# Kernel optimization log

Measured on AMD Instinct MI355X. Metric: run time of the kernel, lower is better.

The kernel has to match this reference:

```python
import jax, jax.numpy as jnp
import numpy as np

N_USERS = 100000
N_ITEMS = 50001  # item_max + 1 (padding row 0)
N_EDGES = 1000000
D = 64
B = 4096
MAXLEN = 50
NUM_GNN_LAYERS = 2
LAMBDA_A = 0.5


def setup_inputs() -> dict:
    key = jax.random.key(0)
    ks = jax.random.split(key, 11)
    user_table = jax.random.normal(ks[0], (N_USERS, D), jnp.float32) * 0.1
    item_table = jax.random.normal(ks[1], (N_ITEMS, D), jnp.float32) * 0.1
    item_table = item_table.at[0].set(0.0)  # padding_idx=0
    edge_val_uv = jax.random.uniform(ks[2], (N_EDGES,), jnp.float32)
    edge_val_vu = jax.random.uniform(ks[3], (N_EDGES,), jnp.float32)
    W_att_w = jax.random.normal(ks[4], (D, D), jnp.float32) / jnp.sqrt(D)
    W_att_b = jax.random.normal(ks[5], (D,), jnp.float32) * 0.01
    W_agg = jax.random.normal(ks[6], (D, D), jnp.float32) / jnp.sqrt(D)
    edge_u = jax.random.randint(ks[7], (N_EDGES,), 0, N_USERS, jnp.int32)
    edge_i = jax.random.randint(ks[8], (N_EDGES,), 0, N_ITEMS, jnp.int32)
    user_idx = jax.random.randint(ks[9], (B,), 0, N_USERS, jnp.int32)
    ctx_items = jax.random.randint(ks[10], (B, MAXLEN), 0, N_ITEMS, jnp.int32)
    return dict(user_table=user_table, item_table=item_table,
                edge_val_uv=edge_val_uv, edge_val_vu=edge_val_vu,
                W_att_w=W_att_w, W_att_b=W_att_b, W_agg=W_agg,
                edge_u=edge_u, edge_i=edge_i, user_idx=user_idx,
                ctx_items=ctx_items)


def _propagate(V0, edge_u, edge_i, edge_val_uv, edge_val_vu):
    # V_{l+1} = VU @ (UV @ V_l), sparse bipartite spmm via segment sums
    V = V0
    layers = [V]
    for _ in range(NUM_GNN_LAYERS):
        u_msg = jax.ops.segment_sum(edge_val_uv[:, None] * V[edge_i],
                                    edge_u, num_segments=N_USERS)  # [U, D]
        V = jax.ops.segment_sum(edge_val_vu[:, None] * u_msg[edge_u],
                                edge_i, num_segments=N_ITEMS)       # [I, D]
        layers.append(V)
    return jnp.mean(jnp.stack(layers, 0), axis=0) + V0


def reference(user_table, item_table, edge_val_uv, edge_val_vu,
              W_att_w, W_att_b, W_agg,
              edge_u, edge_i, user_idx, ctx_items):
    # item_embedding_select: GNN propagation over bipartite graph
    V = _propagate(item_table, edge_u, edge_i, edge_val_uv, edge_val_vu)

    # forward_user
    id_emb = user_table[user_idx]          # [B, D]
    seq_emb = V[ctx_items]                  # [B, L, D]

    # user_attention_pooling
    key = jnp.tanh(jnp.einsum('bld,ed->ble', seq_emb, W_att_w) + W_att_b)
    attention = jnp.einsum('bld,bd->bl', key, id_emb)
    mask = jnp.sum(seq_emb, axis=-1) == 0   # [B, L]
    X = jnp.where(mask, 0.0, attention)
    eX = jnp.exp(X)
    attn = eX / (jnp.sum(eX, axis=1, keepdims=True) + 1e-12)
    pooled = jnp.einsum('bl,bld->bd', attn, seq_emb)
    out = pooled @ W_agg.T

    return LAMBDA_A * id_emb + (1.0 - LAMBDA_A) * out
```

## Files before the change

kernel.cpp:

```cpp
#include <hip/hip_runtime.h>

#define N_USERS 100000
#define N_ITEMS 50001
#define N_EDGES 1000000
#define D 64
#define BATCH 4096
#define MAXLEN 50

#define SHU 8
#define SHI 7
#define NBU ((N_USERS + 255) >> 8)
#define NBI ((N_ITEMS + 127) >> 7)
#define CAP 3072
#define BEPB 8192
#define BBLOCKS ((N_EDGES + BEPB - 1) / BEPB)

typedef __attribute__((ext_vector_type(8))) short short8;
typedef __attribute__((ext_vector_type(4))) float f32x4;

__device__ __forceinline__ float bf_lo(unsigned u) { return __uint_as_float(u << 16); }
__device__ __forceinline__ float bf_hi(unsigned u) { return __uint_as_float(u & 0xffff0000u); }
__device__ __forceinline__ float bf_s(unsigned short s) { return __uint_as_float(((unsigned)s) << 16); }
__device__ __forceinline__ unsigned bf_pack2(float a, float b) {
    unsigned ba = __float_as_uint(a);
    unsigned bb = __float_as_uint(b);
    ba += 0x7fffu + ((ba >> 16) & 1u);
    bb += 0x7fffu + ((bb >> 16) & 1u);
    return (ba >> 16) | (bb & 0xffff0000u);
}
__device__ __forceinline__ float fast_tanh(float x) {
    float e = __expf(2.0f * x);
    return 1.0f - 2.0f * __builtin_amdgcn_rcpf(e + 1.0f);
}

__global__ __launch_bounds__(256) void convert_kernel(
    const float* __restrict__ src, unsigned* __restrict__ dst, int npairs)
{
    int i = blockIdx.x * 256 + threadIdx.x;
    if (i < npairs) {
        float2 f = ((const float2*)src)[i];
        dst[i] = bf_pack2(f.x, f.y);
    }
}

__global__ __launch_bounds__(512) void bin_kernel(
    const int* __restrict__ eu, const int* __restrict__ ei,
    const float* __restrict__ ev_uv, const float* __restrict__ ev_vu,
    int* __restrict__ gcur_u, int* __restrict__ gcur_i,
    int2* __restrict__ staged_u, int2* __restrict__ staged_i)
{
    __shared__ int hist[NBU];
    __shared__ int runbase[NBU];
    __shared__ unsigned short rank[BEPB];
    int tid = threadIdx.x;
    int dir_i = (blockIdx.x >= BBLOCKS) ? 1 : 0;
    int blk = blockIdx.x - (dir_i ? BBLOCKS : 0);
    const int* erow = dir_i ? ei : eu;
    const int* esrc = dir_i ? eu : ei;
    const float* eval = dir_i ? ev_vu : ev_uv;
    int* gcur = dir_i ? gcur_i : gcur_u;
    int2* staged = dir_i ? staged_i : staged_u;
    const int shift = dir_i ? SHI : SHU;
    const float qs = dir_i ? 32767.0f : 65535.0f;
    const int rlmask = dir_i ? 127 : 255;
    const int nb = dir_i ? NBI : NBU;

    for (int i = tid; i < nb; i += 512) hist[i] = 0;
    __syncthreads();
    int e0 = blk * BEPB;
    for (int k = 0; k < BEPB / 512; ++k) {
        int slot = k * 512 + tid;
        int e = e0 + slot;
        if (e < N_EDGES)
            rank[slot] = (unsigned short)atomicAdd(&hist[erow[e] >> shift], 1);
    }
    __syncthreads();
    for (int i = tid; i < nb; i += 512) {
        int cn = hist[i];
        runbase[i] = cn ? (i * CAP + atomicAdd(&gcur[i], cn)) : 0;
    }
    __syncthreads();
    for (int k = 0; k < BEPB / 512; ++k) {
        int slot = k * 512 + tid;
        int e = e0 + slot;
        if (e < N_EDGES) {
            int row = erow[e];
            unsigned q = (unsigned)(fminf(fmaxf(eval[e], 0.0f), 1.0f) * qs + 0.5f);
            int2 en;
            en.x = (int)((unsigned)(row & rlmask) << 16 | q);
            en.y = esrc[e];
            staged[runbase[row >> shift] + rank[slot]] = en;
        }
    }
}

__global__ __launch_bounds__(512) void place_kernel(
    const int2* __restrict__ staged_u, const int2* __restrict__ staged_i,
    const int* __restrict__ gcur_u, const int* __restrict__ gcur_i,
    unsigned* __restrict__ csr_u, unsigned* __restrict__ csr_i,
    int2* __restrict__ offend_u, int2* __restrict__ offend_i)
{
    __shared__ int cnt[256];
    __shared__ int s[256];
    __shared__ int cur[256];
    int tid = threadIdx.x;
    int dir_i = (blockIdx.x >= NBU) ? 1 : 0;
    int b = blockIdx.x - (dir_i ? NBU : 0);
    const int2* staged = dir_i ? staged_i : staged_u;
    const int* gcur = dir_i ? gcur_i : gcur_u;
    unsigned* csr = dir_i ? csr_i : csr_u;
    int2* offend = dir_i ? offend_i : offend_u;
    const int NR = dir_i ? 128 : 256;
    const int nrows = dir_i ? N_ITEMS : N_USERS;
    const int idxbits = dir_i ? 17 : 16;

    int sb = b * CAP;
    int eb = sb + gcur[b];
    if (tid < NR) cnt[tid] = 0;
    __syncthreads();
    for (int idx = sb + tid; idx < eb; idx += 512) {
        int rl = ((unsigned)staged[idx].x) >> 16;
        atomicAdd(&cnt[rl], 1);
    }
    __syncthreads();
    int c = 0;
    if (tid < 256) {
        c = (tid < NR) ? cnt[tid] : 0;
        s[tid] = c;
    }
    __syncthreads();
    for (int off = 1; off < 256; off <<= 1) {
        int v = 0;
        if (tid >= off && tid < 256) v = s[tid - off];
        __syncthreads();
        if (tid < 256) s[tid] += v;
        __syncthreads();
    }
    if (tid < NR) {
        int excl = s[tid] - c;
        int row = b * NR + tid;
        if (row < nrows) {
            int2 oe; oe.x = sb + excl; oe.y = sb + excl + c;
            offend[row] = oe;
        }
        cur[tid] = sb + excl;
    }
    __syncthreads();
    for (int idx = sb + tid; idx < eb; idx += 512) {
        int2 en = staged[idx];
        unsigned w0 = (unsigned)en.x;
        int rl = w0 >> 16;
        unsigned q = w0 & 0xFFFFu;
        int pos = atomicAdd(&cur[rl], 1);
        csr[pos] = (q << idxbits) | (unsigned)en.y;
    }
}

template<int IDXBITS>
__device__ __forceinline__ void gather_row_g8(
    const unsigned* __restrict__ src, const unsigned* __restrict__ csr,
    int o, int e, int c4, int g,
    float& A0, float& A1, float& A2, float& A3,
    float& A4, float& A5, float& A6, float& A7)
{
    constexpr unsigned MASK = (1u << IDXBITS) - 1u;
    constexpr float SCALE = 1.0f / (float)((1u << (32 - IDXBITS)) - 1u);
    float a0 = 0.f, a1 = 0.f, a2 = 0.f, a3 = 0.f;
    float a4 = 0.f, a5 = 0.f, a6 = 0.f, a7 = 0.f;
    for (int base = o; base < e; base += 8) {
        unsigned word = __builtin_nontemporal_load(csr + base + c4);
        uint4 u4[8];
        float v[8];
#pragma unroll
        for (int j = 0; j < 8; ++j) {
            unsigned wj = (unsigned)__shfl((int)word, 8 * g + j, 64);
            bool valid = (base + j) < e;
            int r = valid ? (int)(wj & MASK) : 0;
            v[j] = valid ? (float)(wj >> IDXBITS) * SCALE : 0.0f;
            u4[j] = *(const uint4*)(src + (size_t)r * 32 + 4 * c4);
        }
#pragma unroll
        for (int j = 0; j < 8; ++j) {
            a0 = fmaf(v[j], bf_lo(u4[j].x), a0);
            a1 = fmaf(v[j], bf_hi(u4[j].x), a1);
            a2 = fmaf(v[j], bf_lo(u4[j].y), a2);
            a3 = fmaf(v[j], bf_hi(u4[j].y), a3);
            a4 = fmaf(v[j], bf_lo(u4[j].z), a4);
            a5 = fmaf(v[j], bf_hi(u4[j].z), a5);
            a6 = fmaf(v[j], bf_lo(u4[j].w), a6);
            a7 = fmaf(v[j], bf_hi(u4[j].w), a7);
        }
    }
    A0 = a0; A1 = a1; A2 = a2; A3 = a3;
    A4 = a4; A5 = a5; A6 = a6; A7 = a7;
}

template<int IDXBITS>
__global__ __launch_bounds__(256) void gather_bf_kernel(
    const unsigned* __restrict__ src, const unsigned* __restrict__ csr,
    const int2* __restrict__ offend,
    unsigned* __restrict__ dst, int nrows)
{
    int gw = (blockIdx.x * 256 + threadIdx.x) >> 6;
    int lane = threadIdx.x & 63;
    int g = lane >> 3, c4 = lane & 7;
    int row = gw * 8 + g;
    int2 oe = (row < nrows) ? offend[row] : make_int2(0, 0);
    float a0, a1, a2, a3, a4, a5, a6, a7;
    gather_row_g8<IDXBITS>(src, csr, oe.x, oe.y, c4, g,
                           a0, a1, a2, a3, a4, a5, a6, a7);
    if (row < nrows) {
        uint4 o4;
        o4.x = bf_pack2(a0, a1);
        o4.y = bf_pack2(a2, a3);
        o4.z = bf_pack2(a4, a5);
        o4.w = bf_pack2(a6, a7);
        *((uint4*)(dst + (size_t)row * 32) + c4) = o4;
    }
}

__global__ __launch_bounds__(256) void gather_final_bf_kernel(
    const unsigned* __restrict__ src, const unsigned* __restrict__ csr,
    const int2* __restrict__ offend,
    const float* __restrict__ V0, const unsigned* __restrict__ V1bf,
    unsigned* __restrict__ Vf_bf)
{
    int gw = (blockIdx.x * 256 + threadIdx.x) >> 6;
    int lane = threadIdx.x & 63;
    int g = lane >> 3, c4 = lane & 7;
    int row = gw * 8 + g;
    int2 oe = (row < N_ITEMS) ? offend[row] : make_int2(0, 0);
    float a0, a1, a2, a3, a4, a5, a6, a7;
    gather_row_g8<17>(src, csr, oe.x, oe.y, c4, g,
                      a0, a1, a2, a3, a4, a5, a6, a7);
    if (row < N_ITEMS) {
        float4 v0a = *((const float4*)(V0 + (size_t)row * 64) + 2 * c4);
        float4 v0b = *((const float4*)(V0 + (size_t)row * 64) + 2 * c4 + 1);
        uint4 u1 = *((const uint4*)(V1bf + (size_t)row * 32) + c4);
        float r0 = (v0a.x + bf_lo(u1.x) + a0) * (1.0f / 3.0f) + v0a.x;
        float r1 = (v0a.y + bf_hi(u1.x) + a1) * (1.0f / 3.0f) + v0a.y;
        float r2 = (v0a.z + bf_lo(u1.y) + a2) * (1.0f / 3.0f) + v0a.z;
        float r3 = (v0a.w + bf_hi(u1.y) + a3) * (1.0f / 3.0f) + v0a.w;
        float r4 = (v0b.x + bf_lo(u1.z) + a4) * (1.0f / 3.0f) + v0b.x;
        float r5 = (v0b.y + bf_hi(u1.z) + a5) * (1.0f / 3.0f) + v0b.y;
        float r6 = (v0b.z + bf_lo(u1.w) + a6) * (1.0f / 3.0f) + v0b.z;
        float r7 = (v0b.w + bf_hi(u1.w) + a7) * (1.0f / 3.0f) + v0b.w;
        uint4 o4;
        o4.x = bf_pack2(r0, r1);
        o4.y = bf_pack2(r2, r3);
        o4.z = bf_pack2(r4, r5);
        o4.w = bf_pack2(r6, r7);
        *((uint4*)(Vf_bf + (size_t)row * 32) + c4) = o4;
    }
}

__global__ __launch_bounds__(256) void phase2_kernel(
    const float* __restrict__ user_table, const unsigned* __restrict__ Vf_bf,
    const float* __restrict__ Watt, const float* __restrict__ Wb,
    const float* __restrict__ Wagg, const int* __restrict__ uidx,
    const int* __restrict__ ctx, float* __restrict__ out)
{
    __shared__ __align__(16) unsigned seq[4][50 * 36];
    __shared__ unsigned short wgT[64 * 65];
    __shared__ __align__(16) float idrow[4][64];
    __shared__ float attn_l[4][64];
    __shared__ float pooled_l[4][64];

    const int tid = threadIdx.x;
    const int w = tid >> 6;
    const int lane = tid & 63;
    const int q = lane >> 4;
    const int n = lane & 15;
    const int b = blockIdx.x * 4 + w;

    int ci = (lane < MAXLEN) ? ctx[b * MAXLEN + lane] : 0;
    const int g8 = lane >> 3, c4v = lane & 7;
    uint4 vv[7];
#pragma unroll
    for (int bt = 0; bt < 7; ++bt) {
        int l = bt * 8 + g8;
        int rsrc = __shfl(ci, l, 64);
        vv[bt] = *((const uint4*)(Vf_bf + (size_t)rsrc * 32) + c4v);
    }

    for (int i = tid; i < 64 * 64; i += 256) {
        int e = i >> 6, d = i & 63;
        unsigned bb = __float_as_uint(Wagg[i]);
        bb += 0x7fffu + ((bb >> 16) & 1u);
        wgT[d * 65 + e] = (unsigned short)(bb >> 16);
    }
    __syncthreads();

    short8 wa_f[4][2];
#pragma unroll
    for (int et = 0; et < 4; ++et)
#pragma unroll
        for (int ks = 0; ks < 2; ++ks) {
            const float* rp = Watt + (size_t)(16 * et + n) * 64 + 32 * ks + 8 * q;
            float4 f0 = *(const float4*)rp;
            float4 f1 = *(const float4*)(rp + 4);
            union { short8 s; unsigned u[4]; } t;
            t.u[0] = bf_pack2(f0.x, f0.y);
            t.u[1] = bf_pack2(f0.z, f0.w);
            t.u[2] = bf_pack2(f1.x, f1.y);
            t.u[3] = bf_pack2(f1.z, f1.w);
            wa_f[et][ks] = t.s;
        }
    f32x4 biasv[4];
#pragma unroll
    for (int et = 0; et < 4; ++et)
        biasv[et] = *(const f32x4*)(Wb + 16 * et + 4 * q);
    short8 ones8;
#pragma unroll
    for (int j = 0; j < 8; ++j) ones8[j] = (short)0x3F80;

    int uid = uidx[b];
    idrow[w][lane] = user_table[(size_t)uid * 64 + lane];
    f32x4 idv[4];
#pragma unroll
    for (int et = 0; et < 4; ++et)
        idv[et] = *(f32x4*)&idrow[w][16 * et + 4 * q];

#pragma unroll
    for (int bt = 0; bt < 7; ++bt) {
        int l = bt * 8 + g8;
        if (l < MAXLEN)
            *(uint4*)&seq[w][l * 36 + 4 * c4v] = vv[bt];
    }

    float xs[4];
#pragma unroll
    for (int lt = 0; lt < 4; ++lt) {
        union { short8 s; uint4 u; } B0, B1;
        B0.u = *(const uint4*)&seq[w][(16 * lt + n) * 36 + 4 * q];
        B1.u = *(const uint4*)&seq[w][(16 * lt + n) * 36 + 16 + 4 * q];

        f32x4 rsum = {0.f, 0.f, 0.f, 0.f};
        rsum = __builtin_amdgcn_mfma_f32_16x16x32_bf16(ones8, B0.s, rsum, 0, 0, 0);
        rsum = __builtin_amdgcn_mfma_f32_16x16x32_bf16(ones8, B1.s, rsum, 0, 0, 0);
        float rsv = rsum[0];

        float xacc = 0.0f;
#pragma unroll
        for (int et = 0; et < 4; ++et) {
            f32x4 a = {0.f, 0.f, 0.f, 0.f};
            a = __builtin_amdgcn_mfma_f32_16x16x32_bf16(wa_f[et][0], B0.s, a, 0, 0, 0);
            a = __builtin_amdgcn_mfma_f32_16x16x32_bf16(wa_f[et][1], B1.s, a, 0, 0, 0);
#pragma unroll
            for (int r = 0; r < 4; ++r) {
                float t = fast_tanh(a[r] + biasv[et][r]);
                xacc = fmaf(t, idv[et][r], xacc);
            }
        }
        xacc += __shfl_xor(xacc, 16, 64);
        xacc += __shfl_xor(xacc, 32, 64);
        xs[lt] = (rsv == 0.0f) ? 0.0f : xacc;
    }

    float ex[4];
    float tot = 0.0f;
#pragma unroll
    for (int lt = 0; lt < 4; ++lt) {
        int l = 16 * lt + n;
        ex[lt] = (l < MAXLEN) ? __expf(xs[lt]) : 0.0f;
        tot += ex[lt];
    }
    tot += __shfl_xor(tot, 1, 64);
    tot += __shfl_xor(tot, 2, 64);
    tot += __shfl_xor(tot, 4, 64);
    tot += __shfl_xor(tot, 8, 64);
    float inv = 1.0f / (tot + 1e-12f);
    if (lane < 16) {
#pragma unroll
        for (int lt = 0; lt < 4; ++lt)
            attn_l[w][16 * lt + lane] = ex[lt] * inv;
    }

    float pooled = 0.0f;
    for (int l = 0; l < MAXLEN; ++l) {
        float a = attn_l[w][l];
        unsigned uu = seq[w][l * 36 + (lane >> 1)];
        float sv = (lane & 1) ? bf_hi(uu) : bf_lo(uu);
        pooled = fmaf(a, sv, pooled);
    }
    pooled_l[w][lane] = pooled;

    float o = 0.0f;
#pragma unroll 8
    for (int d = 0; d < 64; ++d) {
        float pv = pooled_l[w][d];
        float wv = bf_s(wgT[d * 65 + lane]);
        o = fmaf(pv, wv, o);
    }
    out[(size_t)b * 64 + lane] = 0.5f * idrow[w][lane] + 0.5f * o;
}


extern "C" void kernel_launch(void* const* d_in, const int* in_sizes, int n_in,
                              void* d_out, int out_size, void* d_ws, size_t ws_size,
                              hipStream_t stream)
{
    const float* user_table = (const float*)d_in[0];
    const float* item_table = (const float*)d_in[1];
    const float* ev_uv      = (const float*)d_in[2];
    const float* ev_vu      = (const float*)d_in[3];
    const float* Watt       = (const float*)d_in[4];
    const float* Wb         = (const float*)d_in[5];
    const float* Wagg       = (const float*)d_in[6];
    const int*   edge_u     = (const int*)d_in[7];
    const int*   edge_i     = (const int*)d_in[8];
    const int*   uidx       = (const int*)d_in[9];
    const int*   ctx        = (const int*)d_in[10];
    float* out = (float*)d_out;

    const size_t NCAP = (size_t)NBU * CAP;

    char* p = (char*)d_ws;
    unsigned* it_bf    = (unsigned*)p; p += (size_t)N_ITEMS * 32 * 4;
    unsigned* u_msg_bf = (unsigned*)p; p += (size_t)N_USERS * 32 * 4;
    unsigned* V1_bf    = (unsigned*)p; p += (size_t)N_ITEMS * 32 * 4;
    char*     Sreg     = p;            p += NCAP * 8 * 2;
    int2*     staged_u = (int2*)Sreg;
    int2*     staged_i = (int2*)(Sreg + NCAP * 8);
    unsigned* Vf_bf    = (unsigned*)Sreg;
    unsigned* csr_u    = (unsigned*)p; p += NCAP * 4;
    unsigned* csr_i    = (unsigned*)p; p += NCAP * 4;
    int2*     offend_u = (int2*)p;     p += (size_t)N_USERS * 8;
    int2*     offend_i = (int2*)p;     p += (size_t)N_ITEMS * 8;
    int*      gcur_u   = (int*)p;      p += NBU * 4;
    int*      gcur_i   = (int*)p;      p += NBI * 4;

    hipMemsetAsync(gcur_u, 0, (NBU + NBI) * 4, stream);

    convert_kernel<<<(N_ITEMS * 32 + 255) / 256, 256, 0, stream>>>(
        item_table, it_bf, N_ITEMS * 32);

    bin_kernel<<<2 * BBLOCKS, 512, 0, stream>>>(edge_u, edge_i, ev_uv, ev_vu,
                                                gcur_u, gcur_i, staged_u, staged_i);
    place_kernel<<<NBU + NBI, 512, 0, stream>>>(staged_u, staged_i, gcur_u, gcur_i,
                                                csr_u, csr_i, offend_u, offend_i);

    const int ublocks = (N_USERS + 31) / 32;
    const int iblocks = (N_ITEMS + 31) / 32;

    gather_bf_kernel<16><<<ublocks, 256, 0, stream>>>(it_bf, csr_u, offend_u, u_msg_bf, N_USERS);
    gather_bf_kernel<17><<<iblocks, 256, 0, stream>>>(u_msg_bf, csr_i, offend_i, V1_bf, N_ITEMS);
    gather_bf_kernel<16><<<ublocks, 256, 0, stream>>>(V1_bf, csr_u, offend_u, u_msg_bf, N_USERS);
    gather_final_bf_kernel<<<iblocks, 256, 0, stream>>>(u_msg_bf, csr_i, offend_i,
                                                        item_table, V1_bf, Vf_bf);

    phase2_kernel<<<BATCH / 4, 256, 0, stream>>>(user_table, Vf_bf, Watt, Wb, Wagg,
                                                 uidx, ctx, out);
}
```

Before: 254.3 us.

## Split CSR rows into source-index chunks to localize gather accesses

The place kernel now buckets each row's edges by source-index range: 2 chunks for user rows and 4 for item rows. Offsets are stored per (row, chunk), and the gather kernels walk the chunks in order. All rows then touch a similar slice of the source table at roughly the same time, which is meant to improve L2/cache locality of the random embedding gathers. The costs are larger offset arrays, partially filled 8-edge groups at every chunk boundary, and a wider 512-entry scan in place_kernel. Phase2 also moves its context-row gather later, after the weight setup, which lowers register pressure but exposes that load's latency.

```diff
diff --git a/kernel.cpp b/kernel.cpp
--- a/kernel.cpp
+++ b/kernel.cpp
@@ -14,6 +14,11 @@
 #define CAP 3072
 #define BEPB 8192
 #define BBLOCKS ((N_EDGES + BEPB - 1) / BEPB)
+
+#define NCH_U 2
+#define NCH_I 4
+#define UCHUNK_SPLIT 25024
+#define ICHUNK_DIV 25000u
 
 typedef __attribute__((ext_vector_type(8))) short short8;
 typedef __attribute__((ext_vector_type(4))) float f32x4;
@@ -100,9 +105,9 @@
     unsigned* __restrict__ csr_u, unsigned* __restrict__ csr_i,
     int2* __restrict__ offend_u, int2* __restrict__ offend_i)
 {
-    __shared__ int cnt[256];
-    __shared__ int s[256];
-    __shared__ int cur[256];
+    __shared__ int cnt[512];
+    __shared__ int s[512];
+    __shared__ int cur[512];
     int tid = threadIdx.x;
     int dir_i = (blockIdx.x >= NBU) ? 1 : 0;
     int b = blockIdx.x - (dir_i ? NBU : 0);
@@ -111,62 +116,66 @@
     unsigned* csr = dir_i ? csr_i : csr_u;
     int2* offend = dir_i ? offend_i : offend_u;
     const int NR = dir_i ? 128 : 256;
+    const int NCH = dir_i ? NCH_I : NCH_U;
     const int nrows = dir_i ? N_ITEMS : N_USERS;
     const int idxbits = dir_i ? 17 : 16;
 
     int sb = b * CAP;
     int eb = sb + gcur[b];
-    if (tid < NR) cnt[tid] = 0;
+    cnt[tid] = 0;
     __syncthreads();
     for (int idx = sb + tid; idx < eb; idx += 512) {
-        int rl = ((unsigned)staged[idx].x) >> 16;
-        atomicAdd(&cnt[rl], 1);
-    }
-    __syncthreads();
-    int c = 0;
-    if (tid < 256) {
-        c = (tid < NR) ? cnt[tid] : 0;
-        s[tid] = c;
-    }
-    __syncthreads();
-    for (int off = 1; off < 256; off <<= 1) {
-        int v = 0;
-        if (tid >= off && tid < 256) v = s[tid - off];
+        int2 en = staged[idx];
+        int rl = ((unsigned)en.x) >> 16;
+        int c = dir_i ? (int)((unsigned)en.y / ICHUNK_DIV)
+                      : (en.y >= UCHUNK_SPLIT ? 1 : 0);
+        atomicAdd(&cnt[rl * NCH + c], 1);
+    }
+    __syncthreads();
+    int cv = cnt[tid];
+    s[tid] = cv;
+    __syncthreads();
+    for (int off = 1; off < 512; off <<= 1) {
+        int v = (tid >= off) ? s[tid - off] : 0;
         __syncthreads();
-        if (tid < 256) s[tid] += v;
+        s[tid] += v;
         __syncthreads();
     }
-    if (tid < NR) {
-        int excl = s[tid] - c;
-        int row = b * NR + tid;
+    int excl = s[tid] - cv;
+    {
+        int rl = tid / NCH;
+        int c = tid - rl * NCH;
+        int row = b * NR + rl;
         if (row < nrows) {
-            int2 oe; oe.x = sb + excl; oe.y = sb + excl + c;
-            offend[row] = oe;
-        }
-        cur[tid] = sb + excl;
-    }
+            int2 oe;
+            oe.x = sb + excl;
+            oe.y = sb + excl + cv;
+            offend[(size_t)row * NCH + c] = oe;
+        }
+    }
+    cur[tid] = sb + excl;
     __syncthreads();
     for (int idx = sb + tid; idx < eb; idx += 512) {
         int2 en = staged[idx];
         unsigned w0 = (unsigned)en.x;
         int rl = w0 >> 16;
         unsigned q = w0 & 0xFFFFu;
-        int pos = atomicAdd(&cur[rl], 1);
+        int c = dir_i ? (int)((unsigned)en.y / ICHUNK_DIV)
+                      : (en.y >= UCHUNK_SPLIT ? 1 : 0);
+        int pos = atomicAdd(&cur[rl * NCH + c], 1);
         csr[pos] = (q << idxbits) | (unsigned)en.y;
     }
 }
 
 template<int IDXBITS>
-__device__ __forceinline__ void gather_row_g8(
+__device__ __forceinline__ void gather_range_g8(
     const unsigned* __restrict__ src, const unsigned* __restrict__ csr,
     int o, int e, int c4, int g,
-    float& A0, float& A1, float& A2, float& A3,
-    float& A4, float& A5, float& A6, float& A7)
+    float& a0, float& a1, float& a2, float& a3,
+    float& a4, float& a5, float& a6, float& a7)
 {
     constexpr unsigned MASK = (1u << IDXBITS) - 1u;
     constexpr float SCALE = 1.0f / (float)((1u << (32 - IDXBITS)) - 1u);
-    float a0 = 0.f, a1 = 0.f, a2 = 0.f, a3 = 0.f;
-    float a4 = 0.f, a5 = 0.f, a6 = 0.f, a7 = 0.f;
     for (int base = o; base < e; base += 8) {
         unsigned word = __builtin_nontemporal_load(csr + base + c4);
         uint4 u4[8];
@@ -191,11 +200,9 @@
             a7 = fmaf(v[j], bf_hi(u4[j].w), a7);
         }
     }
-    A0 = a0; A1 = a1; A2 = a2; A3 = a3;
-    A4 = a4; A5 = a5; A6 = a6; A7 = a7;
-}
-
-template<int IDXBITS>
+}
+
+template<int IDXBITS, int NCH>
 __global__ __launch_bounds__(256) void gather_bf_kernel(
     const unsigned* __restrict__ src, const unsigned* __restrict__ csr,
     const int2* __restrict__ offend,
@@ -205,10 +212,14 @@
     int lane = threadIdx.x & 63;
     int g = lane >> 3, c4 = lane & 7;
     int row = gw * 8 + g;
-    int2 oe = (row < nrows) ? offend[row] : make_int2(0, 0);
-    float a0, a1, a2, a3, a4, a5, a6, a7;
-    gather_row_g8<IDXBITS>(src, csr, oe.x, oe.y, c4, g,
-                           a0, a1, a2, a3, a4, a5, a6, a7);
+    float a0 = 0.f, a1 = 0.f, a2 = 0.f, a3 = 0.f;
+    float a4 = 0.f, a5 = 0.f, a6 = 0.f, a7 = 0.f;
+#pragma unroll
+    for (int c = 0; c < NCH; ++c) {
+        int2 oe = (row < nrows) ? offend[(size_t)row * NCH + c] : make_int2(0, 0);
+        gather_range_g8<IDXBITS>(src, csr, oe.x, oe.y, c4, g,
+                                 a0, a1, a2, a3, a4, a5, a6, a7);
+    }
     if (row < nrows) {
         uint4 o4;
         o4.x = bf_pack2(a0, a1);
@@ -229,10 +240,14 @@
     int lane = threadIdx.x & 63;
     int g = lane >> 3, c4 = lane & 7;
     int row = gw * 8 + g;
-    int2 oe = (row < N_ITEMS) ? offend[row] : make_int2(0, 0);
-    float a0, a1, a2, a3, a4, a5, a6, a7;
-    gather_row_g8<17>(src, csr, oe.x, oe.y, c4, g,
-                      a0, a1, a2, a3, a4, a5, a6, a7);
+    float a0 = 0.f, a1 = 0.f, a2 = 0.f, a3 = 0.f;
+    float a4 = 0.f, a5 = 0.f, a6 = 0.f, a7 = 0.f;
+#pragma unroll
+    for (int c = 0; c < NCH_I; ++c) {
+        int2 oe = (row < N_ITEMS) ? offend[(size_t)row * NCH_I + c] : make_int2(0, 0);
+        gather_range_g8<17>(src, csr, oe.x, oe.y, c4, g,
+                            a0, a1, a2, a3, a4, a5, a6, a7);
+    }
     if (row < N_ITEMS) {
         float4 v0a = *((const float4*)(V0 + (size_t)row * 64) + 2 * c4);
         float4 v0b = *((const float4*)(V0 + (size_t)row * 64) + 2 * c4 + 1);
@@ -273,16 +288,6 @@
     const int n = lane & 15;
     const int b = blockIdx.x * 4 + w;
 
-    int ci = (lane < MAXLEN) ? ctx[b * MAXLEN + lane] : 0;
-    const int g8 = lane >> 3, c4v = lane & 7;
-    uint4 vv[7];
-#pragma unroll
-    for (int bt = 0; bt < 7; ++bt) {
-        int l = bt * 8 + g8;
-        int rsrc = __shfl(ci, l, 64);
-        vv[bt] = *((const uint4*)(Vf_bf + (size_t)rsrc * 32) + c4v);
-    }
-
     for (int i = tid; i < 64 * 64; i += 256) {
         int e = i >> 6, d = i & 63;
         unsigned bb = __float_as_uint(Wagg[i]);
@@ -321,11 +326,17 @@
     for (int et = 0; et < 4; ++et)
         idv[et] = *(f32x4*)&idrow[w][16 * et + 4 * q];
 
-#pragma unroll
-    for (int bt = 0; bt < 7; ++bt) {
-        int l = bt * 8 + g8;
-        if (l < MAXLEN)
-            *(uint4*)&seq[w][l * 36 + 4 * c4v] = vv[bt];
+    int ci = (lane < MAXLEN) ? ctx[b * MAXLEN + lane] : 0;
+    {
+        int g8 = lane >> 3, c4 = lane & 7;
+#pragma unroll
+        for (int bt = 0; bt < 7; ++bt) {
+            int l = bt * 8 + g8;
+            int rsrc = __shfl(ci, l, 64);
+            uint4 vv = *((const uint4*)(Vf_bf + (size_t)rsrc * 32) + c4);
+            if (l < MAXLEN)
+                *(uint4*)&seq[w][l * 36 + 4 * c4] = vv;
+        }
     }
 
     float xs[4];
@@ -425,8 +436,8 @@
     unsigned* Vf_bf    = (unsigned*)Sreg;
     unsigned* csr_u    = (unsigned*)p; p += NCAP * 4;
     unsigned* csr_i    = (unsigned*)p; p += NCAP * 4;
-    int2*     offend_u = (int2*)p;     p += (size_t)N_USERS * 8;
-    int2*     offend_i = (int2*)p;     p += (size_t)N_ITEMS * 8;
+    int2*     offend_u = (int2*)p;     p += (size_t)N_USERS * NCH_U * 8;
+    int2*     offend_i = (int2*)p;     p += (size_t)N_ITEMS * NCH_I * 8;
     int*      gcur_u   = (int*)p;      p += NBU * 4;
     int*      gcur_i   = (int*)p;      p += NBI * 4;
 
@@ -443,11 +454,14 @@
     const int ublocks = (N_USERS + 31) / 32;
     const int iblocks = (N_ITEMS + 31) / 32;
 
-    gather_bf_kernel<16><<<ublocks, 256, 0, stream>>>(it_bf, csr_u, offend_u, u_msg_bf, N_USERS);
-    gather_bf_kernel<17><<<iblocks, 256, 0, stream>>>(u_msg_bf, csr_i, offend_i, V1_bf, N_ITEMS);
-    gather_bf_kernel<16><<<ublocks, 256, 0, stream>>>(V1_bf, csr_u, offend_u, u_msg_bf, N_USERS);
-    gather_final_bf_kernel<<<iblocks, 256, 0, stream>>>(u_msg_bf, csr_i, offend_i,
-                                                        item_table, V1_bf, Vf_bf);
+    gather_bf_kernel<16, NCH_U><<<ublocks, 256, 0, stream>>>(
+        it_bf, csr_u, offend_u, u_msg_bf, N_USERS);
+    gather_bf_kernel<17, NCH_I><<<iblocks, 256, 0, stream>>>(
+        u_msg_bf, csr_i, offend_i, V1_bf, N_ITEMS);
+    gather_bf_kernel<16, NCH_U><<<ublocks, 256, 0, stream>>>(
+        V1_bf, csr_u, offend_u, u_msg_bf, N_USERS);
+    gather_final_bf_kernel<<<iblocks, 256, 0, stream>>>(
+        u_msg_bf, csr_i, offend_i, item_table, V1_bf, Vf_bf);
 
     phase2_kernel<<<BATCH / 4, 256, 0, stream>>>(user_table, Vf_bf, Watt, Wb, Wagg,
                                                  uidx, ctx, out);
```

Result: no change. 257.4 us (+1.2%).
